# Kernel optimization log

Measured on AMD Instinct MI355X. Metric: run time of the kernel, lower is better.

## Reference

```python
import jax, jax.numpy as jnp
import numpy as np

B, L, HC, D = 4, 4096, 4, 1024
K, DIL = 4, 2
EPS = 1e-5
C = HC * D
PAD = (K - 1) * DIL


def setup_inputs() -> dict:
    key = jax.random.key(0)
    k1, k2, k3 = jax.random.split(key, 3)
    x = jax.random.normal(k1, (B, L, HC, D), dtype=jnp.float32)
    # RMSNorm affine weights, one per chunk (torch init: ones; randomize slightly for a
    # non-trivial baseline)
    norm_weight = 1.0 + 0.02 * jax.random.normal(k2, (HC, D), dtype=jnp.float32)
    # depthwise conv weight [C, 1, K] (torch init is zeros; use small random values so
    # the kernel-correctness baseline is non-degenerate)
    conv_weight = 0.1 * jax.random.normal(k3, (C, 1, K), dtype=jnp.float32)
    return {"x": x, "norm_weight": norm_weight, "conv_weight": conv_weight}


def reference(x, norm_weight, conv_weight):
    # per-chunk RMSNorm over last dim: [B, L, HC, D]
    ms = jnp.mean(jnp.square(x), axis=-1, keepdims=True)
    xn = x * jax.lax.rsqrt(ms + EPS) * norm_weight[None, None, :, :]
    # concat chunks along feature dim -> [B, L, C], then to [B, C, L]
    xc = xn.reshape(B, L, C).transpose(0, 2, 1)
    # depthwise dilated causal conv1d: left-pad (K-1)*DIL, output length L
    y = jax.lax.conv_general_dilated(
        xc, conv_weight,
        window_strides=(1,),
        padding=((PAD, 0),),
        rhs_dilation=(DIL,),
        feature_group_count=C,
        dimension_numbers=("NCH", "OIH", "NCH"),
    )
    y = jax.nn.silu(y)
    # back to [B, L, HC, D]
    return y.transpose(0, 2, 1).reshape(B, L, HC, D)
```

## Files before the change

### kernel.cpp

```cpp
#include <hip/hip_runtime.h>

namespace {

constexpr int NB = 4, L = 4096, HC = 4, D = 1024, KW = 4;
constexpr int PAD = 6;
constexpr float EPS = 1e-5f;
constexpr int ST = 4;
constexpr int NSTEP = 16;
constexpr int CL = ST * NSTEP;
constexpr int NT = L / CL;
constexpr int BDIM = 256;

typedef float f32x4 __attribute__((ext_vector_type(4)));

#define LGKM_BARRIER() do {                                    \
    asm volatile("s_waitcnt lgkmcnt(0)" ::: "memory");         \
    __builtin_amdgcn_s_barrier();                              \
} while (0)

__device__ __forceinline__ void stage16(const float* g, float* l) {
    __builtin_amdgcn_global_load_lds(
        (const __attribute__((address_space(1))) void*)g,
        (__attribute__((address_space(3))) void*)l, 16, 0, 0);
}

__global__ __launch_bounds__(BDIM, 4) void engram_shortconv_tri(
    const float* __restrict__ x,
    const float* __restrict__ nw,
    const float* __restrict__ cw,
    float* __restrict__ out)
{
    __shared__ float s_buf[3][ST][D];
    __shared__ float s_inv[2][ST];
    __shared__ float s_invh[PAD];

    const int lblk = (blockIdx.x & 7) * 128 + (blockIdx.x >> 3);
    const int t    = lblk % NT;
    const int hc   = (lblk / NT) % HC;
    const int b    = lblk / (NT * HC);
    const int l0   = t * CL;

    const int tid  = threadIdx.x;
    const int wave = tid >> 6;
    const int lane = tid & 63;

    const size_t rs = (size_t)HC * D;
    const float* xbase = x + ((size_t)b * L * HC + (size_t)hc) * D;
    const float* xcol  = xbase + tid * 4;
    float*       ocol  = out + ((size_t)b * L * HC + (size_t)hc) * D + tid * 4;

    #pragma unroll
    for (int s = 0; s < 3; ++s)
        #pragma unroll
        for (int r = 0; r < ST; ++r)
            stage16(xcol + (size_t)(l0 + s * ST + r) * rs, &s_buf[s][r][wave * 256]);

    const float4 nw4 = *(const float4*)(nw + (size_t)hc * D + tid * 4);
    float4 cwv[4];
    #pragma unroll
    for (int j = 0; j < 4; ++j)
        cwv[j] = *(const float4*)(cw + ((size_t)hc * D + tid * 4 + j) * KW);

    float win[PAD][4];
    #pragma unroll
    for (int r = 0; r < PAD; ++r) {
        const int l = l0 - PAD + r;
        float4 v = make_float4(0.f, 0.f, 0.f, 0.f);
        if (l >= 0) v = *(const float4*)(xcol + (size_t)l * rs);
        win[r][0] = v.x; win[r][1] = v.y; win[r][2] = v.z; win[r][3] = v.w;
    }

    #pragma unroll
    for (int rr = wave; rr < PAD; rr += 4) {
        const int l = l0 - PAD + rr;
        float ss = 0.0f;
        if (l >= 0) {
            const float* rp = xbase + (size_t)l * rs;
            #pragma unroll
            for (int q = 0; q < 4; ++q) {
                const f32x4 v = *(const f32x4*)(rp + lane * 4 + q * 256);
                ss = fmaf(v.x, v.x, fmaf(v.y, v.y, fmaf(v.z, v.z, fmaf(v.w, v.w, ss))));
            }
        }
        #pragma unroll
        for (int off = 32; off >= 1; off >>= 1) ss += __shfl_xor(ss, off);
        if (lane == 0) s_invh[rr] = rsqrtf(ss * (1.0f / D) + EPS);
    }

    float wk[4][4];
    {
        const float gv[4] = { nw4.x, nw4.y, nw4.z, nw4.w };
        #pragma unroll
        for (int j = 0; j < 4; ++j) {
            wk[j][0] = cwv[j].x * gv[j]; wk[j][1] = cwv[j].y * gv[j];
            wk[j][2] = cwv[j].z * gv[j]; wk[j][3] = cwv[j].w * gv[j];
        }
    }

    LGKM_BARRIER();
    #pragma unroll
    for (int r = 0; r < PAD; ++r) {
        const float iv = s_invh[r];
        win[r][0] *= iv; win[r][1] *= iv; win[r][2] *= iv; win[r][3] *= iv;
    }
    asm volatile("s_waitcnt vmcnt(0)" ::: "memory");
    __builtin_amdgcn_s_barrier();
    {
        const int row = wave;
        float ss = 0.0f;
        #pragma unroll
        for (int q = 0; q < 4; ++q) {
            const f32x4 v = *(const f32x4*)&s_buf[0][row][lane * 4 + q * 256];
            ss = fmaf(v.x, v.x, fmaf(v.y, v.y, fmaf(v.z, v.z, fmaf(v.w, v.w, ss))));
        }
        #pragma unroll
        for (int off = 32; off >= 1; off >>= 1) ss += __shfl_xor(ss, off);
        if (lane == 0) s_inv[0][row] = rsqrtf(ss * (1.0f / D) + EPS);
    }
    LGKM_BARRIER();

    #pragma unroll
    for (int s = 0; s < NSTEP; ++s) {
        if (s < NSTEP - 1) {
            const int row = wave;
            const float* rp = &s_buf[(s + 1) % 3][row][0];
            float ss = 0.0f;
            #pragma unroll
            for (int q = 0; q < 4; ++q) {
                const f32x4 v = *(const f32x4*)(rp + lane * 4 + q * 256);
                ss = fmaf(v.x, v.x, fmaf(v.y, v.y, fmaf(v.z, v.z, fmaf(v.w, v.w, ss))));
            }
            #pragma unroll
            for (int off = 32; off >= 1; off >>= 1) ss += __shfl_xor(ss, off);
            if (lane == 0) s_inv[(s + 1) & 1][row] = rsqrtf(ss * (1.0f / D) + EPS);
        }

        const int base = l0 + s * ST;
        float cur[ST][4];
        #pragma unroll
        for (int r = 0; r < ST; ++r) {
            const f32x4 v = *(const f32x4*)&s_buf[s % 3][r][tid * 4];
            const float iv = s_inv[s & 1][r];
            cur[r][0] = v.x * iv; cur[r][1] = v.y * iv;
            cur[r][2] = v.z * iv; cur[r][3] = v.w * iv;
        }
        #pragma unroll
        for (int i = 0; i < ST; ++i) {
            float av[4];
            #pragma unroll
            for (int j = 0; j < 4; ++j) {
                float a = 0.0f;
                #pragma unroll
                for (int k = 0; k < 4; ++k) {
                    const int rel = i - 6 + 2 * k;
                    const float xv = (rel < 0) ? win[6 + rel][j] : cur[rel][j];
                    a = fmaf(wk[j][k], xv, a);
                }
                av[j] = a / (1.0f + __expf(-a));
            }
            f32x4 o = { av[0], av[1], av[2], av[3] };
            *(f32x4*)(ocol + (size_t)(base + i) * rs) = o;
        }

        win[0][0]=win[4][0]; win[0][1]=win[4][1]; win[0][2]=win[4][2]; win[0][3]=win[4][3];
        win[1][0]=win[5][0]; win[1][1]=win[5][1]; win[1][2]=win[5][2]; win[1][3]=win[5][3];
        #pragma unroll
        for (int r = 0; r < ST; ++r) {
            win[2 + r][0] = cur[r][0]; win[2 + r][1] = cur[r][1];
            win[2 + r][2] = cur[r][2]; win[2 + r][3] = cur[r][3];
        }

        if (s < NSTEP - 3) {
            asm volatile("s_waitcnt lgkmcnt(0)" ::: "memory");
            __builtin_amdgcn_sched_barrier(0);
            #pragma unroll
            for (int r = 0; r < ST; ++r)
                stage16(xcol + (size_t)(l0 + (s + 3) * ST + r) * rs,
                        &s_buf[s % 3][r][wave * 256]);
            __builtin_amdgcn_sched_barrier(0);
        }

        if (s <= NSTEP - 4)      asm volatile("s_waitcnt vmcnt(8)" ::: "memory");
        else if (s == NSTEP - 3) asm volatile("s_waitcnt vmcnt(4)" ::: "memory");
        if (s < NSTEP - 1) LGKM_BARRIER();
    }
}

}

extern "C" void kernel_launch(void* const* d_in, const int* in_sizes, int n_in,
                              void* d_out, int out_size, void* d_ws, size_t ws_size,
                              hipStream_t stream) {
    const float* x  = (const float*)d_in[0];
    const float* nw = (const float*)d_in[1];
    const float* cw = (const float*)d_in[2];
    float* out = (float*)d_out;

    const int nblocks = NB * HC * NT;
    engram_shortconv_tri<<<dim3(nblocks), dim3(BDIM), 0, stream>>>(x, nw, cw, out);
}
```

Before: 111.8 us.

## Halve rows per pipeline step, compute halo norms from registers, use nontemporal stores

Cuts rows per step from 4 to 2 with 32 steps per tile and rotates the triple buffer with pointers in a non-unrolled loop. Halo RMS norms are now computed from the already-loaded window registers through an LDS partial-sum reduction instead of re-reading global memory. Output stores become nontemporal and are issued after the prefetch, with the vmcnt waits adjusted to match. The aim is smaller code, shallower waits and no redundant halo loads, at the cost of more barriers per row.

```diff
diff --git a/kernel.cpp b/kernel.cpp
--- a/kernel.cpp
+++ b/kernel.cpp
@@ -5,8 +5,8 @@
 constexpr int NB = 4, L = 4096, HC = 4, D = 1024, KW = 4;
 constexpr int PAD = 6;
 constexpr float EPS = 1e-5f;
-constexpr int ST = 4;
-constexpr int NSTEP = 16;
+constexpr int ST = 2;
+constexpr int NSTEP = 32;
 constexpr int CL = ST * NSTEP;
 constexpr int NT = L / CL;
 constexpr int BDIM = 256;
@@ -24,14 +24,15 @@
         (__attribute__((address_space(3))) void*)l, 16, 0, 0);
 }
 
-__global__ __launch_bounds__(BDIM, 4) void engram_shortconv_tri(
+__global__ __launch_bounds__(BDIM, 4) void engram_shortconv_v9(
     const float* __restrict__ x,
     const float* __restrict__ nw,
     const float* __restrict__ cw,
     float* __restrict__ out)
 {
     __shared__ float s_buf[3][ST][D];
-    __shared__ float s_inv[2][ST];
+    __shared__ float s_part[PAD][BDIM];
+    __shared__ float s_inv2[2][ST];
     __shared__ float s_invh[PAD];
 
     const int lblk = (blockIdx.x & 7) * 128 + (blockIdx.x >> 3);
@@ -45,15 +46,8 @@
     const int lane = tid & 63;
 
     const size_t rs = (size_t)HC * D;
-    const float* xbase = x + ((size_t)b * L * HC + (size_t)hc) * D;
-    const float* xcol  = xbase + tid * 4;
-    float*       ocol  = out + ((size_t)b * L * HC + (size_t)hc) * D + tid * 4;
-
-    #pragma unroll
-    for (int s = 0; s < 3; ++s)
-        #pragma unroll
-        for (int r = 0; r < ST; ++r)
-            stage16(xcol + (size_t)(l0 + s * ST + r) * rs, &s_buf[s][r][wave * 256]);
+    const float* xcol = x   + ((size_t)b * L * HC + (size_t)hc) * D + tid * 4;
+    float*       ocol = out + ((size_t)b * L * HC + (size_t)hc) * D + tid * 4;
 
     const float4 nw4 = *(const float4*)(nw + (size_t)hc * D + tid * 4);
     float4 cwv[4];
@@ -71,82 +65,98 @@
     }
 
     #pragma unroll
-    for (int rr = wave; rr < PAD; rr += 4) {
-        const int l = l0 - PAD + rr;
+    for (int s = 0; s < 3; ++s)
+        #pragma unroll
+        for (int r = 0; r < ST; ++r)
+            stage16(xcol + (size_t)(l0 + s * ST + r) * rs, &s_buf[s][r][wave * 256]);
+
+    float wk[4][4];
+    {
+        const float gv[4] = { nw4.x, nw4.y, nw4.z, nw4.w };
+        #pragma unroll
+        for (int j = 0; j < 4; ++j) {
+            wk[j][0] = cwv[j].x * gv[j]; wk[j][1] = cwv[j].y * gv[j];
+            wk[j][2] = cwv[j].z * gv[j]; wk[j][3] = cwv[j].w * gv[j];
+        }
+    }
+
+    #pragma unroll
+    for (int r = 0; r < PAD; ++r)
+        s_part[r][tid] = win[r][0]*win[r][0] + win[r][1]*win[r][1]
+                       + win[r][2]*win[r][2] + win[r][3]*win[r][3];
+    LGKM_BARRIER();
+    {
+        int rr = wave;
+        float s1 = s_part[rr][lane]       + s_part[rr][lane + 64]
+                 + s_part[rr][lane + 128] + s_part[rr][lane + 192];
+        #pragma unroll
+        for (int off = 32; off >= 1; off >>= 1) s1 += __shfl_xor(s1, off);
+        if (lane == 0) s_invh[rr] = rsqrtf(s1 * (1.0f / D) + EPS);
+        rr = wave + 4;
+        if (rr < PAD) {
+            float s2 = s_part[rr][lane]       + s_part[rr][lane + 64]
+                     + s_part[rr][lane + 128] + s_part[rr][lane + 192];
+            #pragma unroll
+            for (int off = 32; off >= 1; off >>= 1) s2 += __shfl_xor(s2, off);
+            if (lane == 0) s_invh[rr] = rsqrtf(s2 * (1.0f / D) + EPS);
+        }
+    }
+    LGKM_BARRIER();
+    #pragma unroll
+    for (int r = 0; r < PAD; ++r) {
+        const float iv = s_invh[r];
+        win[r][0] *= iv; win[r][1] *= iv; win[r][2] *= iv; win[r][3] *= iv;
+    }
+
+    asm volatile("s_waitcnt vmcnt(2)" ::: "memory");
+    __builtin_amdgcn_s_barrier();
+    {
+        const int row = wave & 1;
+        const float* rp = &s_buf[0][row][0];
         float ss = 0.0f;
-        if (l >= 0) {
-            const float* rp = xbase + (size_t)l * rs;
+        #pragma unroll
+        for (int q = 0; q < 4; ++q) {
+            const f32x4 v = *(const f32x4*)(rp + lane * 4 + q * 256);
+            ss = fmaf(v.x, v.x, fmaf(v.y, v.y, fmaf(v.z, v.z, fmaf(v.w, v.w, ss))));
+        }
+        #pragma unroll
+        for (int off = 32; off >= 1; off >>= 1) ss += __shfl_xor(ss, off);
+        if (lane == 0) s_inv2[0][row] = rsqrtf(ss * (1.0f / D) + EPS);
+    }
+    LGKM_BARRIER();
+
+    float* p0 = &s_buf[0][0][0];
+    float* p1 = &s_buf[1][0][0];
+    float* p2 = &s_buf[2][0][0];
+
+    #pragma unroll 1
+    for (int s = 0; s < NSTEP; ++s) {
+        if (s < NSTEP - 1) {
+            const int row = wave & 1;
+            const float* rp = p1 + row * D;
+            float ss = 0.0f;
             #pragma unroll
             for (int q = 0; q < 4; ++q) {
                 const f32x4 v = *(const f32x4*)(rp + lane * 4 + q * 256);
                 ss = fmaf(v.x, v.x, fmaf(v.y, v.y, fmaf(v.z, v.z, fmaf(v.w, v.w, ss))));
             }
-        }
-        #pragma unroll
-        for (int off = 32; off >= 1; off >>= 1) ss += __shfl_xor(ss, off);
-        if (lane == 0) s_invh[rr] = rsqrtf(ss * (1.0f / D) + EPS);
-    }
-
-    float wk[4][4];
-    {
-        const float gv[4] = { nw4.x, nw4.y, nw4.z, nw4.w };
-        #pragma unroll
-        for (int j = 0; j < 4; ++j) {
-            wk[j][0] = cwv[j].x * gv[j]; wk[j][1] = cwv[j].y * gv[j];
-            wk[j][2] = cwv[j].z * gv[j]; wk[j][3] = cwv[j].w * gv[j];
-        }
-    }
-
-    LGKM_BARRIER();
-    #pragma unroll
-    for (int r = 0; r < PAD; ++r) {
-        const float iv = s_invh[r];
-        win[r][0] *= iv; win[r][1] *= iv; win[r][2] *= iv; win[r][3] *= iv;
-    }
-    asm volatile("s_waitcnt vmcnt(0)" ::: "memory");
-    __builtin_amdgcn_s_barrier();
-    {
-        const int row = wave;
-        float ss = 0.0f;
-        #pragma unroll
-        for (int q = 0; q < 4; ++q) {
-            const f32x4 v = *(const f32x4*)&s_buf[0][row][lane * 4 + q * 256];
-            ss = fmaf(v.x, v.x, fmaf(v.y, v.y, fmaf(v.z, v.z, fmaf(v.w, v.w, ss))));
-        }
-        #pragma unroll
-        for (int off = 32; off >= 1; off >>= 1) ss += __shfl_xor(ss, off);
-        if (lane == 0) s_inv[0][row] = rsqrtf(ss * (1.0f / D) + EPS);
-    }
-    LGKM_BARRIER();
-
-    #pragma unroll
-    for (int s = 0; s < NSTEP; ++s) {
-        if (s < NSTEP - 1) {
-            const int row = wave;
-            const float* rp = &s_buf[(s + 1) % 3][row][0];
-            float ss = 0.0f;
-            #pragma unroll
-            for (int q = 0; q < 4; ++q) {
-                const f32x4 v = *(const f32x4*)(rp + lane * 4 + q * 256);
-                ss = fmaf(v.x, v.x, fmaf(v.y, v.y, fmaf(v.z, v.z, fmaf(v.w, v.w, ss))));
-            }
             #pragma unroll
             for (int off = 32; off >= 1; off >>= 1) ss += __shfl_xor(ss, off);
-            if (lane == 0) s_inv[(s + 1) & 1][row] = rsqrtf(ss * (1.0f / D) + EPS);
+            if (lane == 0) s_inv2[(s + 1) & 1][row] = rsqrtf(ss * (1.0f / D) + EPS);
         }
 
         const int base = l0 + s * ST;
         float cur[ST][4];
         #pragma unroll
         for (int r = 0; r < ST; ++r) {
-            const f32x4 v = *(const f32x4*)&s_buf[s % 3][r][tid * 4];
-            const float iv = s_inv[s & 1][r];
+            const f32x4 v = *(const f32x4*)(p0 + r * D + tid * 4);
+            const float iv = s_inv2[s & 1][r];
             cur[r][0] = v.x * iv; cur[r][1] = v.y * iv;
             cur[r][2] = v.z * iv; cur[r][3] = v.w * iv;
         }
+        float ov[ST][4];
         #pragma unroll
         for (int i = 0; i < ST; ++i) {
-            float av[4];
             #pragma unroll
             for (int j = 0; j < 4; ++j) {
                 float a = 0.0f;
@@ -156,18 +166,19 @@
                     const float xv = (rel < 0) ? win[6 + rel][j] : cur[rel][j];
                     a = fmaf(wk[j][k], xv, a);
                 }
-                av[j] = a / (1.0f + __expf(-a));
+                ov[i][j] = a / (1.0f + __expf(-a));
             }
-            f32x4 o = { av[0], av[1], av[2], av[3] };
-            *(f32x4*)(ocol + (size_t)(base + i) * rs) = o;
-        }
-
-        win[0][0]=win[4][0]; win[0][1]=win[4][1]; win[0][2]=win[4][2]; win[0][3]=win[4][3];
-        win[1][0]=win[5][0]; win[1][1]=win[5][1]; win[1][2]=win[5][2]; win[1][3]=win[5][3];
+        }
+
+        #pragma unroll
+        for (int r = 0; r < PAD - ST; ++r) {
+            win[r][0] = win[r + ST][0]; win[r][1] = win[r + ST][1];
+            win[r][2] = win[r + ST][2]; win[r][3] = win[r + ST][3];
+        }
         #pragma unroll
         for (int r = 0; r < ST; ++r) {
-            win[2 + r][0] = cur[r][0]; win[2 + r][1] = cur[r][1];
-            win[2 + r][2] = cur[r][2]; win[2 + r][3] = cur[r][3];
+            win[PAD - ST + r][0] = cur[r][0]; win[PAD - ST + r][1] = cur[r][1];
+            win[PAD - ST + r][2] = cur[r][2]; win[PAD - ST + r][3] = cur[r][3];
         }
 
         if (s < NSTEP - 3) {
@@ -176,13 +187,23 @@
             #pragma unroll
             for (int r = 0; r < ST; ++r)
                 stage16(xcol + (size_t)(l0 + (s + 3) * ST + r) * rs,
-                        &s_buf[s % 3][r][wave * 256]);
+                        p0 + r * D + wave * 256);
             __builtin_amdgcn_sched_barrier(0);
         }
 
-        if (s <= NSTEP - 4)      asm volatile("s_waitcnt vmcnt(8)" ::: "memory");
-        else if (s == NSTEP - 3) asm volatile("s_waitcnt vmcnt(4)" ::: "memory");
-        if (s < NSTEP - 1) LGKM_BARRIER();
+        #pragma unroll
+        for (int i = 0; i < ST; ++i) {
+            f32x4 o = { ov[i][0], ov[i][1], ov[i][2], ov[i][3] };
+            __builtin_nontemporal_store(o, (f32x4*)(ocol + (size_t)(base + i) * rs));
+        }
+
+        if (s < NSTEP - 1) {
+            if (s <= NSTEP - 4)      asm volatile("s_waitcnt vmcnt(6)" ::: "memory");
+            else if (s == NSTEP - 3) asm volatile("s_waitcnt vmcnt(4)" ::: "memory");
+            LGKM_BARRIER();
+        }
+
+        float* tmp = p0; p0 = p1; p1 = p2; p2 = tmp;
     }
 }
 
@@ -197,5 +218,5 @@
     float* out = (float*)d_out;
 
     const int nblocks = NB * HC * NT;
-    engram_shortconv_tri<<<dim3(nblocks), dim3(BDIM), 0, stream>>>(x, nw, cw, out);
-}
+    engram_shortconv_v9<<<dim3(nblocks), dim3(BDIM), 0, stream>>>(x, nw, cw, out);
+}
```

Result: faster. 96.85 us (-13.4%).
